# Kernel tuning notes

Hardware: AMD Instinct MI355X
Metric: run time of the kernel (lower is better)

The kernel has to match this reference:

```python
import jax, jax.numpy as jnp
import numpy as np

NUM_HEADS = 8


def _mab(Q, K, Wq, bq, Wk, bk, Wv, bv, Wo, bo):
    # MAB with ln=False, dropout=0 (eval). Scale is sqrt(dim_V), matching source.
    B, Lq, _ = Q.shape
    Lk = K.shape[1]
    Dv = Wq.shape[1]
    dh = Dv // NUM_HEADS
    q = (Q @ Wq + bq).reshape(B, Lq, NUM_HEADS, dh).transpose(0, 2, 1, 3)
    k = (K @ Wk + bk).reshape(B, Lk, NUM_HEADS, dh).transpose(0, 2, 1, 3)
    v = (K @ Wv + bv).reshape(B, Lk, NUM_HEADS, dh).transpose(0, 2, 1, 3)
    A = jax.nn.softmax(jnp.einsum('bhqd,bhkd->bhqk', q, k) / jnp.sqrt(jnp.float32(Dv)), axis=-1)
    O = (q + jnp.einsum('bhqk,bhkd->bhqd', A, v)).transpose(0, 2, 1, 3).reshape(B, Lq, Dv)
    return O + jax.nn.relu(O @ Wo + bo)


def _forward(x, adj, gin_W, gin_b, geW1, geb1, geW2, geb2,
             gnW1, gnb1, gnW2, gnb2, goW, gob, S,
             mWq, mbq, mWk, mbk, mWv, mbv, mWo, mbo, finW, finb):
    B, V, T, D = x.shape
    Hd = gin_W.shape[1]
    # --- GNN encoder (adj path) ---
    h = x.reshape(B, V, T * D) @ gin_W + gin_b            # [B,V,H]
    # edge_mlp first linear on cat([h_i,h_j]) == h@Wi (row) + h@Wj (col); avoids 2H concat
    Wi, Wj = geW1[:Hd], geW1[Hd:]
    pre = (h @ Wi)[:, :, None, :] + (h @ Wj)[:, None, :, :] + geb1   # [B,V,V,H]
    e = jax.nn.relu(jax.nn.relu(pre) @ geW2 + geb2)       # [B,V,V,H]
    agg = jnp.einsum('bijh,bij->bih', e, adj)             # mask * sum over j, fused
    node = jax.nn.relu(jax.nn.relu(agg @ gnW1 + gnb1) @ gnW2 + gnb2)
    enc = node @ goW + gob                                # [B,V,H]
    # --- decoder: PMA + SAB + SAB + Linear ---
    o = _mab(jnp.broadcast_to(S, (B,) + S.shape[1:]), enc,
             mWq[0], mbq[0], mWk[0], mbk[0], mWv[0], mbv[0], mWo[0], mbo[0])
    o = _mab(o, o, mWq[1], mbq[1], mWk[1], mbk[1], mWv[1], mbv[1], mWo[1], mbo[1])
    o = _mab(o, o, mWq[2], mbq[2], mWk[2], mbk[2], mWv[2], mbv[2], mWo[2], mbo[2])
    out = o @ finW + finb                                 # [B,num_slots,T*OD]
    return out.reshape(B, S.shape[1], T, finW.shape[1] // T)


def setup_inputs() -> dict:
    key = jax.random.key(0)
    ks = jax.random.split(key, 16)
    B, V, T, D = 4, 256, 12, 4
    H, NS, OD = 256, 16, 32

    def w(k, shape, s=0.02):
        return s * jax.random.normal(k, shape, jnp.float32)

    return {
        'x': jax.random.normal(ks[0], (B, V, T, D), jnp.float32),
        'adj': (jax.random.uniform(ks[1], (B, V, V)) > 0.5).astype(jnp.float32),
        'gin_W': w(ks[2], (T * D, H)), 'gin_b': jnp.zeros((H,), jnp.float32),
        'geW1': w(ks[3], (2 * H, H)), 'geb1': jnp.zeros((H,), jnp.float32),
        'geW2': w(ks[4], (H, H)), 'geb2': jnp.zeros((H,), jnp.float32),
        'gnW1': w(ks[5], (H, H)), 'gnb1': jnp.zeros((H,), jnp.float32),
        'gnW2': w(ks[6], (H, H)), 'gnb2': jnp.zeros((H,), jnp.float32),
        'goW': w(ks[7], (H, H)), 'gob': jnp.zeros((H,), jnp.float32),
        'S': w(ks[8], (1, NS, H), 0.05),
        'mWq': w(ks[9], (3, H, H)), 'mbq': jnp.zeros((3, H), jnp.float32),
        'mWk': w(ks[10], (3, H, H)), 'mbk': jnp.zeros((3, H), jnp.float32),
        'mWv': w(ks[11], (3, H, H)), 'mbv': jnp.zeros((3, H), jnp.float32),
        'mWo': w(ks[12], (3, H, H)), 'mbo': jnp.zeros((3, H), jnp.float32),
        'finW': w(ks[13], (H, T * OD)), 'finb': jnp.zeros((T * OD,), jnp.float32),
    }


def reference(x, adj, gin_W, gin_b, geW1, geb1, geW2, geb2,
              gnW1, gnb1, gnW2, gnb2, goW, gob, S,
              mWq, mbq, mWk, mbk, mWv, mbv, mWo, mbo, finW, finb):
    return _forward(x, adj, gin_W, gin_b, geW1, geb1, geW2, geb2,
                    gnW1, gnb1, gnW2, gnb2, goW, gob, S,
                    mWq, mbq, mWk, mbk, mWv, mbv, mWo, mbo, finW, finb)
```

## Files before the change

### kernel.cpp

```cpp
#include <hip/hip_runtime.h>
#include <hip/hip_bf16.h>

typedef unsigned short u16;
typedef __bf16 bf8v __attribute__((ext_vector_type(8)));
typedef float f4v __attribute__((ext_vector_type(4)));

__device__ __forceinline__ float b2f(u16 v) {
  union { unsigned u; float f; } x; x.u = ((unsigned)v) << 16; return x.f;
}
__device__ __forceinline__ u16 f2b(float f) {
  union { float f; unsigned u; } x; x.f = f;
  unsigned r = (x.u + 0x7FFFu + ((x.u >> 16) & 1u)) >> 16;
  return (u16)r;
}
__device__ __forceinline__ unsigned pkbf(float a, float b) {
  union { __hip_bfloat162 h; unsigned u; } c;
  c.h = __float22bfloat162_rn(make_float2(a, b));
  return c.u;
}
__device__ __forceinline__ void up2(unsigned u, float& lo, float& hi) {
  union { unsigned x; float f; } a, b;
  a.x = u << 16; b.x = u & 0xffff0000u; lo = a.f; hi = b.f;
}

#define NFRAG 19
struct PreArgs {
  const float* fsrc[NFRAG];
  u16* fdst[NFRAG];
  int fstride[NFRAG];
  int fbase[NFRAG + 1];
  int fragTiles, hBase, prepBid, q1Bid;
  const float *x, *ginW, *ginb;
  u16* h_bf;
  const float *mbk, *mbv, *mbq, *S, *mWq;
  float *bkv0, *bqkv1, *bqkv2;
  u16* q1b;
};

__global__ __launch_bounds__(256) void k_pre(PreArgs a) {
  __shared__ u16 ld[256 * 20];
  __shared__ float xs[4][48];
  __shared__ float Ss[4096];
  const int bid = blockIdx.x, t = threadIdx.x;

  if (bid < a.fragTiles) {
    int j = 0;
    while (j + 1 < NFRAG && a.fbase[j + 1] <= bid) j++;
    const int localT = bid - a.fbase[j];
    const float* src = a.fsrc[j];
    const int Ns = a.fstride[j];
    const int n0 = localT * 16;
    {
      const float* s = src + (size_t)t * Ns + n0;
      const float4 v0 = ((const float4*)s)[0], v1 = ((const float4*)s)[1];
      const float4 v2 = ((const float4*)s)[2], v3 = ((const float4*)s)[3];
      unsigned* row = (unsigned*)(ld + t * 20);
      row[0] = pkbf(v0.x, v0.y); row[1] = pkbf(v0.z, v0.w);
      row[2] = pkbf(v1.x, v1.y); row[3] = pkbf(v1.z, v1.w);
      row[4] = pkbf(v2.x, v2.y); row[5] = pkbf(v2.z, v2.w);
      row[6] = pkbf(v3.x, v3.y); row[7] = pkbf(v3.z, v3.w);
    }
    __syncthreads();
    u16* dst = a.fdst[j] + (size_t)localT * 4096;
#pragma unroll
    for (int s2 = 0; s2 < 2; s2++) {
      const int o = t * 2 + s2, kt = o >> 6, lane = o & 63;
      const int nlo = lane & 15, bk = kt * 32 + ((lane >> 4) << 3);
      union { u16 h[8]; uint4 q; } pk;
#pragma unroll
      for (int j2 = 0; j2 < 8; j2++) pk.h[j2] = ld[(bk + j2) * 20 + nlo];
      *(uint4*)(dst + (size_t)(kt * 64 + lane) * 8) = pk.q;
    }
    return;
  }
  if (bid >= a.hBase && bid < a.hBase + 256) {
    const int row0 = (bid - a.hBase) * 4;
    if (t < 192) {
      const int rr = t / 48, k = t % 48;
      xs[rr][k] = a.x[(size_t)(row0 + rr) * 48 + k];
    }
    __syncthreads();
    const float bias = a.ginb[t];
    float acc[4] = {bias, bias, bias, bias};
    for (int k = 0; k < 48; k++) {
      const float w = a.ginW[(size_t)k * 256 + t];
#pragma unroll
      for (int rr = 0; rr < 4; rr++) acc[rr] += xs[rr][k] * w;
    }
#pragma unroll
    for (int rr = 0; rr < 4; rr++) a.h_bf[(size_t)(row0 + rr) * 256 + t] = f2b(acc[rr]);
    return;
  }
  if (bid == a.prepBid) {
    a.bkv0[t] = a.mbk[t]; a.bkv0[256 + t] = a.mbv[t];
    a.bqkv1[t] = a.mbq[256 + t]; a.bqkv1[256 + t] = a.mbk[256 + t]; a.bqkv1[512 + t] = a.mbv[256 + t];
    a.bqkv2[t] = a.mbq[512 + t]; a.bqkv2[256 + t] = a.mbk[512 + t]; a.bqkv2[512 + t] = a.mbv[512 + t];
    return;
  }
  if (bid == a.q1Bid) {
    for (int idx = t; idx < 4096; idx += 256) Ss[idx] = a.S[idx];
    __syncthreads();
    float acc[16];
#pragma unroll
    for (int r = 0; r < 16; r++) acc[r] = 0.f;
    for (int k = 0; k < 256; k++) {
      const float w = a.mWq[(size_t)k * 256 + t];
#pragma unroll
      for (int r = 0; r < 16; r++) acc[r] += Ss[r * 256 + k] * w;
    }
    const float bq = a.mbq[t];
#pragma unroll
    for (int r = 0; r < 16; r++) a.q1b[r * 256 + t] = f2b(acc[r] + bq);
    return;
  }
}

__global__ __launch_bounds__(256) void k_wiwj(
    const u16* __restrict__ h, const u16* __restrict__ frag,
    float* __restrict__ hWiF, u16* __restrict__ hWjB) {
  __shared__ __align__(16) u16 As[64 * 264];
  const int t = threadIdx.x, lane = t & 63, wv = t >> 6;
  const int m0 = blockIdx.x * 64, n0 = blockIdx.y * 128;
  {
    const int row = t >> 2, ch = t & 3;
#pragma unroll
    for (int s = 0; s < 8; s++)
      *(uint4*)(As + row * 264 + ch * 64 + s * 8) =
          *(const uint4*)(h + (size_t)(m0 + row) * 256 + ch * 64 + s * 8);
  }
  __syncthreads();
  f4v acc[4][2];
#pragma unroll
  for (int mt = 0; mt < 4; mt++)
#pragma unroll
    for (int nt = 0; nt < 2; nt++) acc[mt][nt] = (f4v){0.f, 0.f, 0.f, 0.f};
  const int Tw = (n0 >> 4) + wv * 2;
#pragma unroll
  for (int kt = 0; kt < 8; kt++) {
    bf8v af[4], bf[2];
#pragma unroll
    for (int mt = 0; mt < 4; mt++)
      af[mt] = *(const bf8v*)(As + (mt * 16 + (lane & 15)) * 264 + kt * 32 + ((lane >> 4) << 3));
#pragma unroll
    for (int nt = 0; nt < 2; nt++)
      bf[nt] = *(const bf8v*)(frag + ((size_t)((Tw + nt) * 8 + kt) * 64 + lane) * 8);
#pragma unroll
    for (int mt = 0; mt < 4; mt++)
#pragma unroll
      for (int nt = 0; nt < 2; nt++)
        acc[mt][nt] = __builtin_amdgcn_mfma_f32_16x16x32_bf16(af[mt], bf[nt], acc[mt][nt], 0, 0, 0);
  }
#pragma unroll
  for (int mt = 0; mt < 4; mt++)
#pragma unroll
    for (int nt = 0; nt < 2; nt++) {
      const int n = n0 + wv * 32 + nt * 16 + (lane & 15);
      const int mb = m0 + mt * 16 + ((lane >> 4) << 2);
#pragma unroll
      for (int r = 0; r < 4; r++) {
        if (n < 256)
          hWiF[(size_t)(mb + r) * 256 + n] = acc[mt][nt][r];
        else
          hWjB[(size_t)(mb + r) * 256 + (n - 256)] = f2b(acc[mt][nt][r]);
      }
    }
}

__global__ __launch_bounds__(256) void k_edge(
    const float* __restrict__ hWiF, const u16* __restrict__ hWjB,
    const float* __restrict__ adj, const float* __restrict__ geb1,
    const u16* __restrict__ fragW2, const float* __restrict__ geb2,
    u16* __restrict__ aggB) {
  __shared__ __align__(16) u16 As[64 * 280];
  __shared__ float hi[256];
  __shared__ int jlist[256];
  __shared__ int cnt;
  const int t = threadIdx.x, lane = t & 63, wv = t >> 6;
  const int b = blockIdx.x >> 8, i = blockIdx.x & 255;
  if (t == 0) cnt = 0;
  __syncthreads();
  {
    const float a = adj[(size_t)(b * 256 + i) * 256 + t];
    hi[t] = hWiF[(size_t)(b * 256 + i) * 256 + t] + geb1[t];
    if (a != 0.f) { const int p = atomicAdd(&cnt, 1); jlist[p] = t; }
  }
  __syncthreads();
  const int nact = cnt;
  if (nact == 0) {
    if (lane < 16) {
#pragma unroll
      for (int nt = 0; nt < 4; nt++)
        aggB[(size_t)(b * 256 + i) * 256 + wv * 64 + nt * 16 + lane] = 0;
    }
    return;
  }
  const int nch = (nact + 63) >> 6;
  float bias2[4];
#pragma unroll
  for (int nt = 0; nt < 4; nt++) bias2[nt] = geb2[wv * 64 + nt * 16 + (lane & 15)];
  float aggAcc[4] = {0.f, 0.f, 0.f, 0.f};
  const u16* fw = fragW2 + lane * 8;
  const int r = t >> 2, q = t & 3;

  uint4 G[8];
  {
    const int rows0 = min(64, nact);
    const int j = (r < rows0) ? jlist[r] : jlist[0];
    const uint4* s4 = (const uint4*)(hWjB + (size_t)(b * 256 + j) * 256 + q * 64);
#pragma unroll
    for (int ii = 0; ii < 8; ii++) G[ii] = s4[ii];
  }

  for (int c = 0; c < nch; c++) {
    const int rows = min(64, nact - c * 64);
    {
      u16* dstrow = As + r * 280 + q * 72;
#pragma unroll
      for (int ii = 0; ii < 8; ii++) {
        const uint4 v = G[ii];
        const int k = q * 64 + ii * 8;
        float f0, f1, f2, f3, f4, f5, f6, f7;
        up2(v.x, f0, f1); up2(v.y, f2, f3); up2(v.z, f4, f5); up2(v.w, f6, f7);
        uint4 qd;
        qd.x = pkbf(fmaxf(f0 + hi[k + 0], 0.f), fmaxf(f1 + hi[k + 1], 0.f));
        qd.y = pkbf(fmaxf(f2 + hi[k + 2], 0.f), fmaxf(f3 + hi[k + 3], 0.f));
        qd.z = pkbf(fmaxf(f4 + hi[k + 4], 0.f), fmaxf(f5 + hi[k + 5], 0.f));
        qd.w = pkbf(fmaxf(f6 + hi[k + 6], 0.f), fmaxf(f7 + hi[k + 7], 0.f));
        *(uint4*)(dstrow + ii * 8) = qd;
      }
    }
    __syncthreads();
    if (c + 1 < nch) {
      const int rowsN = min(64, nact - (c + 1) * 64);
      const int j = (r < rowsN) ? jlist[(c + 1) * 64 + r] : jlist[0];
      const uint4* s4 = (const uint4*)(hWjB + (size_t)(b * 256 + j) * 256 + q * 64);
#pragma unroll
      for (int ii = 0; ii < 8; ii++) G[ii] = s4[ii];
    }
    f4v acc[4][4];
#pragma unroll
    for (int jt = 0; jt < 4; jt++)
#pragma unroll
      for (int nt = 0; nt < 4; nt++) acc[jt][nt] = (f4v){0.f, 0.f, 0.f, 0.f};
#pragma unroll
    for (int kt = 0; kt < 8; kt++) {
      bf8v af[4];
      const int coff = (kt >> 1) * 72 + (kt & 1) * 32 + ((lane >> 4) << 3);
#pragma unroll
      for (int jt = 0; jt < 4; jt++)
        af[jt] = *(const bf8v*)(As + (jt * 16 + (lane & 15)) * 280 + coff);
#pragma unroll
      for (int nt = 0; nt < 4; nt++) {
        const bf8v bw = *(const bf8v*)(fw + (size_t)((wv * 4 + nt) * 8 + kt) * 512);
#pragma unroll
        for (int jt = 0; jt < 4; jt++)
          acc[jt][nt] = __builtin_amdgcn_mfma_f32_16x16x32_bf16(af[jt], bw, acc[jt][nt], 0, 0, 0);
      }
    }
    const int rbase = (lane >> 4) * 4;
#pragma unroll
    for (int nt = 0; nt < 4; nt++) {
      float s = 0.f;
#pragma unroll
      for (int jt = 0; jt < 4; jt++) {
        const int r0 = jt * 16 + rbase;
#pragma unroll
        for (int rr = 0; rr < 4; rr++) {
          const float e = fmaxf(acc[jt][nt][rr] + bias2[nt], 0.f);
          s += (r0 + rr < rows) ? e : 0.f;
        }
      }
      s += __shfl_xor(s, 16);
      s += __shfl_xor(s, 32);
      aggAcc[nt] += s;
    }
    __syncthreads();
  }
  if (lane < 16) {
#pragma unroll
    for (int nt = 0; nt < 4; nt++) {
      const int n = wv * 64 + nt * 16 + lane;
      aggB[(size_t)(b * 256 + i) * 256 + n] = f2b(aggAcc[nt]);
    }
  }
}

#define NBLK 32

__device__ __forceinline__ void gridbar(int* cnt, int gen) {
  __syncthreads();
  if (threadIdx.x == 0) {
    __threadfence();
    __hip_atomic_fetch_add(cnt, 1, __ATOMIC_RELAXED, __HIP_MEMORY_SCOPE_AGENT);
    int it = 0;
    while (__hip_atomic_load(cnt, __ATOMIC_RELAXED, __HIP_MEMORY_SCOPE_AGENT) < NBLK * gen) {
      __builtin_amdgcn_s_sleep(8);
      if (((++it) & 255) == 0)
        __hip_atomic_fetch_add(cnt, 0, __ATOMIC_RELAXED, __HIP_MEMORY_SCOPE_AGENT);
    }
    __threadfence();
  }
  __syncthreads();
}

__device__ void g32(const u16* Al, const u16* frag, const float* bias, int relu,
                    u16* Ol, int t) {
  const int lane = t & 63, wv = t >> 6;
  f4v acc[2][4];
#pragma unroll
  for (int mt = 0; mt < 2; mt++)
#pragma unroll
    for (int nt = 0; nt < 4; nt++) acc[mt][nt] = (f4v){0.f, 0.f, 0.f, 0.f};
#pragma unroll
  for (int kt = 0; kt < 8; kt++) {
    bf8v af[2], bf[4];
#pragma unroll
    for (int mt = 0; mt < 2; mt++)
      af[mt] = *(const bf8v*)(Al + (mt * 16 + (lane & 15)) * 264 + kt * 32 + ((lane >> 4) << 3));
#pragma unroll
    for (int nt = 0; nt < 4; nt++)
      bf[nt] = *(const bf8v*)(frag + ((size_t)((wv * 4 + nt) * 8 + kt) * 64 + lane) * 8);
#pragma unroll
    for (int mt = 0; mt < 2; mt++)
#pragma unroll
      for (int nt = 0; nt < 4; nt++)
        acc[mt][nt] = __builtin_amdgcn_mfma_f32_16x16x32_bf16(af[mt], bf[nt], acc[mt][nt], 0, 0, 0);
  }
#pragma unroll
  for (int mt = 0; mt < 2; mt++)
#pragma unroll
    for (int nt = 0; nt < 4; nt++) {
      const int col = wv * 64 + nt * 16 + (lane & 15);
      const float bv = bias[col];
#pragma unroll
      for (int r = 0; r < 4; r++) {
        const int row = mt * 16 + ((lane >> 4) << 2) + r;
        float v = acc[mt][nt][r] + bv;
        if (relu) v = fmaxf(v, 0.f);
        Ol[row * 264 + col] = f2b(v);
      }
    }
}

__device__ void g32kv(const u16* Al, const u16* frag, const float* bias,
                      u16* outG, int t) {
  const int lane = t & 63, wv = t >> 6;
  f4v acc[2][8];
#pragma unroll
  for (int mt = 0; mt < 2; mt++)
#pragma unroll
    for (int nt = 0; nt < 8; nt++) acc[mt][nt] = (f4v){0.f, 0.f, 0.f, 0.f};
#pragma unroll
  for (int kt = 0; kt < 8; kt++) {
    bf8v af[2];
#pragma unroll
    for (int mt = 0; mt < 2; mt++)
      af[mt] = *(const bf8v*)(Al + (mt * 16 + (lane & 15)) * 264 + kt * 32 + ((lane >> 4) << 3));
#pragma unroll
    for (int nt = 0; nt < 8; nt++) {
      const bf8v bf = *(const bf8v*)(frag + ((size_t)((wv * 8 + nt) * 8 + kt) * 64 + lane) * 8);
#pragma unroll
      for (int mt = 0; mt < 2; mt++)
        acc[mt][nt] = __builtin_amdgcn_mfma_f32_16x16x32_bf16(af[mt], bf, acc[mt][nt], 0, 0, 0);
    }
  }
#pragma unroll
  for (int mt = 0; mt < 2; mt++)
#pragma unroll
    for (int nt = 0; nt < 8; nt++) {
      const int col = wv * 128 + nt * 16 + (lane & 15);
      const float bv = bias[col];
#pragma unroll
      for (int r = 0; r < 4; r++) {
        const int row = mt * 16 + ((lane >> 4) << 2) + r;
        outG[(size_t)row * 512 + col] = f2b(acc[mt][nt][r] + bv);
      }
    }
}

__device__ void attn_tile(const u16* __restrict__ qbuf,
                          const u16* __restrict__ kbuf, const u16* __restrict__ vbuf,
                          float* __restrict__ oF, u16* __restrict__ oB,
                          int b, int hd, float* qs, float* sc, float* vs, int t) {
  const int lane = t & 63, wv = t >> 6;
  const int Lk = 256;
  if (t < 64) {
    const int row = t >> 2, part = t & 3;
    const uint4 q4 = *(const uint4*)(qbuf + (size_t)row * 256 + hd * 32 + part * 8);
    float f0, f1, f2, f3, f4, f5, f6, f7;
    up2(q4.x, f0, f1); up2(q4.y, f2, f3); up2(q4.z, f4, f5); up2(q4.w, f6, f7);
    float4* d = (float4*)(qs + row * 32 + part * 8);
    d[0] = make_float4(f0, f1, f2, f3);
    d[1] = make_float4(f4, f5, f6, f7);
  }
  __syncthreads();
  {
    float kv[32];
    const uint4* kp = (const uint4*)(kbuf + (size_t)(b * Lk + t) * 512 + hd * 32);
#pragma unroll
    for (int c4 = 0; c4 < 4; c4++) {
      const uint4 k4 = kp[c4];
      up2(k4.x, kv[c4 * 8 + 0], kv[c4 * 8 + 1]);
      up2(k4.y, kv[c4 * 8 + 2], kv[c4 * 8 + 3]);
      up2(k4.z, kv[c4 * 8 + 4], kv[c4 * 8 + 5]);
      up2(k4.w, kv[c4 * 8 + 6], kv[c4 * 8 + 7]);
    }
    for (int r = 0; r < 16; r++) {
      float s = 0.f;
#pragma unroll
      for (int d = 0; d < 32; d++) s += qs[r * 32 + d] * kv[d];
      sc[r * 256 + t] = s * 0.0625f;
    }
  }
  __syncthreads();
  for (int r = wv * 4; r < wv * 4 + 4; r++) {
    float v[4];
    float mx = -1e30f;
#pragma unroll
    for (int q2 = 0; q2 < 4; q2++) {
      v[q2] = sc[r * 256 + lane + q2 * 64];
      mx = fmaxf(mx, v[q2]);
    }
    for (int off = 32; off; off >>= 1) mx = fmaxf(mx, __shfl_xor(mx, off));
    float sum = 0.f;
#pragma unroll
    for (int q2 = 0; q2 < 4; q2++) { v[q2] = __expf(v[q2] - mx); sum += v[q2]; }
    for (int off = 32; off; off >>= 1) sum += __shfl_xor(sum, off);
    const float inv = 1.f / sum;
#pragma unroll
    for (int q2 = 0; q2 < 4; q2++) sc[r * 256 + lane + q2 * 64] = v[q2] * inv;
  }
  __syncthreads();
  for (int u = t; u < 1024; u += 256) {
    const int row = u >> 2, part = u & 3;
    const uint4 v4 = *(const uint4*)(vbuf + (size_t)(b * Lk + row) * 512 + hd * 32 + part * 8);
    float f0, f1, f2, f3, f4, f5, f6, f7;
    up2(v4.x, f0, f1); up2(v4.y, f2, f3); up2(v4.z, f4, f5); up2(v4.w, f6, f7);
    float4* d = (float4*)(vs + row * 32 + part * 8);
    d[0] = make_float4(f0, f1, f2, f3);
    d[1] = make_float4(f4, f5, f6, f7);
  }
  __syncthreads();
  const int r0 = t >> 5, d = t & 31;
  float a0 = qs[r0 * 32 + d], a1 = qs[(r0 + 8) * 32 + d];
#pragma unroll 4
  for (int j = 0; j < Lk; j++) {
    const float vv = vs[j * 32 + d];
    a0 += sc[r0 * 256 + j] * vv;
    a1 += sc[(r0 + 8) * 256 + j] * vv;
  }
  const int c0 = hd * 32 + d;
  oF[(size_t)(b * 16 + r0) * 256 + c0] = a0;
  oB[(size_t)(b * 16 + r0) * 256 + c0] = f2b(a0);
  oF[(size_t)(b * 16 + r0 + 8) * 256 + c0] = a1;
  oB[(size_t)(b * 16 + r0 + 8) * 256 + c0] = f2b(a1);
}

__device__ void wprojG(const u16* __restrict__ o1b, const float* __restrict__ o1f,
                       const u16* __restrict__ frag, const float* __restrict__ bias,
                       u16* actL, float* residL, int b, int T, int lane) {
  f4v acc = (f4v){0.f, 0.f, 0.f, 0.f};
  const u16* abase = o1b + (size_t)(b * 16 + (lane & 15)) * 256 + ((lane >> 4) << 3);
  const u16* fbase = frag + ((size_t)(T * 8) * 64 + lane) * 8;
#pragma unroll
  for (int kt = 0; kt < 8; kt++)
    acc = __builtin_amdgcn_mfma_f32_16x16x32_bf16(*(const bf8v*)(abase + kt * 32),
                                                  *(const bf8v*)(fbase + (size_t)kt * 512), acc, 0, 0, 0);
  const int col = T * 16 + (lane & 15);
  const float bv = bias[col];
#pragma unroll
  for (int r = 0; r < 4; r++) {
    const int row = ((lane >> 4) << 2) + r;
    const float v = fmaxf(acc[r] + bv, 0.f) + o1f[(size_t)(b * 16 + row) * 256 + col];
    residL[row * 256 + col] = v;
    actL[row * 264 + col] = f2b(v);
  }
}

__device__ void wprojQ(const u16* actL, const u16* __restrict__ frag,
                       const float* __restrict__ bias, u16* qkvL, int T, int lane) {
  f4v acc = (f4v){0.f, 0.f, 0.f, 0.f};
  const u16* abase = actL + (lane & 15) * 264 + ((lane >> 4) << 3);
  const u16* fbase = frag + ((size_t)(T * 8) * 64 + lane) * 8;
#pragma unroll
  for (int kt = 0; kt < 8; kt++)
    acc = __builtin_amdgcn_mfma_f32_16x16x32_bf16(*(const bf8v*)(abase + kt * 32),
                                                  *(const bf8v*)(fbase + (size_t)kt * 512), acc, 0, 0, 0);
  const int col = T * 16 + (lane & 15);
  const float bv = bias[col];
#pragma unroll
  for (int r = 0; r < 4; r++) {
    const int row = ((lane >> 4) << 2) + r;
    qkvL[row * 776 + col] = f2b(acc[r] + bv);
  }
}

__device__ void wprojR(const u16* actIn, const u16* __restrict__ frag,
                       const float* __restrict__ bias, u16* actOut, float* residL,
                       int T, int lane) {
  f4v acc = (f4v){0.f, 0.f, 0.f, 0.f};
  const u16* abase = actIn + (lane & 15) * 264 + ((lane >> 4) << 3);
  const u16* fbase = frag + ((size_t)(T * 8) * 64 + lane) * 8;
#pragma unroll
  for (int kt = 0; kt < 8; kt++)
    acc = __builtin_amdgcn_mfma_f32_16x16x32_bf16(*(const bf8v*)(abase + kt * 32),
                                                  *(const bf8v*)(fbase + (size_t)kt * 512), acc, 0, 0, 0);
  const int col = T * 16 + (lane & 15);
  const float bv = bias[col];
#pragma unroll
  for (int r = 0; r < 4; r++) {
    const int row = ((lane >> 4) << 2) + r;
    const float v = fmaxf(acc[r] + bv, 0.f) + residL[row * 256 + col];
    residL[row * 256 + col] = v;
    actOut[row * 264 + col] = f2b(v);
  }
}

__device__ void wprojF(const u16* actL, const u16* __restrict__ frag,
                       const float* __restrict__ bias, float* __restrict__ outG,
                       int T, int lane) {
  f4v acc = (f4v){0.f, 0.f, 0.f, 0.f};
  const u16* abase = actL + (lane & 15) * 264 + ((lane >> 4) << 3);
  const u16* fbase = frag + ((size_t)(T * 8) * 64 + lane) * 8;
#pragma unroll
  for (int kt = 0; kt < 8; kt++)
    acc = __builtin_amdgcn_mfma_f32_16x16x32_bf16(*(const bf8v*)(abase + kt * 32),
                                                  *(const bf8v*)(fbase + (size_t)kt * 512), acc, 0, 0, 0);
  const int col = T * 16 + (lane & 15);
  const float bv = bias[col];
#pragma unroll
  for (int r = 0; r < 4; r++) {
    const int row = ((lane >> 4) << 2) + r;
    outG[(size_t)row * 384 + col] = acc[r] + bv;
  }
}

__device__ void attnB(const u16* qkvL, float* residL, u16* actOut, float* ps,
                      int hd, int lane) {
  const int r = lane & 15, cg = lane >> 4;
  float qv[32];
  {
    const uint4* qp = (const uint4*)(qkvL + r * 776 + hd * 32);
#pragma unroll
    for (int c4 = 0; c4 < 4; c4++) {
      const uint4 q4 = qp[c4];
      up2(q4.x, qv[c4 * 8 + 0], qv[c4 * 8 + 1]);
      up2(q4.y, qv[c4 * 8 + 2], qv[c4 * 8 + 3]);
      up2(q4.z, qv[c4 * 8 + 4], qv[c4 * 8 + 5]);
      up2(q4.w, qv[c4 * 8 + 6], qv[c4 * 8 + 7]);
    }
  }
  float p[4];
#pragma unroll
  for (int c = 0; c < 4; c++) {
    const int cc = cg * 4 + c;
    const uint4* kp = (const uint4*)(qkvL + cc * 776 + 256 + hd * 32);
    float s = 0.f;
#pragma unroll
    for (int c4 = 0; c4 < 4; c4++) {
      const uint4 k4 = kp[c4];
      float k0, k1;
      up2(k4.x, k0, k1); s += qv[c4 * 8 + 0] * k0 + qv[c4 * 8 + 1] * k1;
      up2(k4.y, k0, k1); s += qv[c4 * 8 + 2] * k0 + qv[c4 * 8 + 3] * k1;
      up2(k4.z, k0, k1); s += qv[c4 * 8 + 4] * k0 + qv[c4 * 8 + 5] * k1;
      up2(k4.w, k0, k1); s += qv[c4 * 8 + 6] * k0 + qv[c4 * 8 + 7] * k1;
    }
    p[c] = s * 0.0625f;
  }
  float mx = fmaxf(fmaxf(p[0], p[1]), fmaxf(p[2], p[3]));
  mx = fmaxf(mx, __shfl_xor(mx, 16));
  mx = fmaxf(mx, __shfl_xor(mx, 32));
  float sum = 0.f;
#pragma unroll
  for (int c = 0; c < 4; c++) { p[c] = __expf(p[c] - mx); sum += p[c]; }
  sum += __shfl_xor(sum, 16);
  sum += __shfl_xor(sum, 32);
  const float inv = 1.f / sum;
#pragma unroll
  for (int c = 0; c < 4; c++) ps[r * 16 + cg * 4 + c] = p[c] * inv;
  float o[8];
#pragma unroll
  for (int j = 0; j < 8; j++) o[j] = qv[cg * 8 + j];
#pragma unroll
  for (int c = 0; c < 16; c++) {
    const float pv = ps[r * 16 + c];
    const uint4 v4 = *(const uint4*)(qkvL + c * 776 + 512 + hd * 32 + cg * 8);
    float v0, v1;
    up2(v4.x, v0, v1); o[0] += pv * v0; o[1] += pv * v1;
    up2(v4.y, v0, v1); o[2] += pv * v0; o[3] += pv * v1;
    up2(v4.z, v0, v1); o[4] += pv * v0; o[5] += pv * v1;
    up2(v4.w, v0, v1); o[6] += pv * v0; o[7] += pv * v1;
  }
  const int col0 = hd * 32 + cg * 8;
#pragma unroll
  for (int j = 0; j < 8; j++) residL[r * 256 + col0 + j] = o[j];
  unsigned* ob = (unsigned*)(actOut + r * 264 + col0);
  ob[0] = pkbf(o[0], o[1]); ob[1] = pkbf(o[2], o[3]);
  ob[2] = pkbf(o[4], o[5]); ob[3] = pkbf(o[6], o[7]);
}

struct TailArgs {
  const u16 *agg, *fGn1, *fGn2, *fGo, *fKV0, *fQKV1, *fQKV2, *fO0, *fO1, *fO2, *fFin, *q1b;
  const float *gnb1, *gnb2, *gob, *bkv0, *bqkv1, *bqkv2, *mbo, *finb;
  u16 *kv1, *o1b;
  float *o1f, *outF;
  int* bar;
};

__global__ __launch_bounds__(256) void k_tail(TailArgs a) {
  __shared__ __align__(16) char smem[62208];
  const int bid = blockIdx.x, t = threadIdx.x;
  const int lane = t & 63, w = t >> 6;

  {
    u16* actA = (u16*)smem;
    u16* actB = (u16*)(smem + 16896);
    const int r0 = bid * 32;
#pragma unroll
    for (int s = 0; s < 4; s++) {
      const int u = t * 4 + s, row = u >> 5, ch = u & 31;
      *(uint4*)(actA + row * 264 + ch * 8) =
          *(const uint4*)(a.agg + (size_t)(r0 + row) * 256 + ch * 8);
    }
    __syncthreads();
    g32(actA, a.fGn1, a.gnb1, 1, actB, t); __syncthreads();
    g32(actB, a.fGn2, a.gnb2, 1, actA, t); __syncthreads();
    g32(actA, a.fGo, a.gob, 0, actB, t); __syncthreads();
    g32kv(actB, a.fKV0, a.bkv0, a.kv1 + (size_t)r0 * 512, t);
  }
  gridbar(a.bar, 1);
  {
    float* qs = (float*)smem;
    float* sc = (float*)(smem + 2048);
    float* vs = (float*)(smem + 18432);
    attn_tile(a.q1b, a.kv1, a.kv1 + 256, a.o1f, a.o1b, bid >> 3, bid & 7, qs, sc, vs, t);
  }
  gridbar(a.bar, 2);
  if (bid >= 4) return;
  {
    const int b = bid;
    u16* act0 = (u16*)smem;
    u16* act1 = (u16*)(smem + 8448);
    u16* qkvL = (u16*)(smem + 16896);
    float* residL = (float*)(smem + 41728);
    float* psL = (float*)(smem + 58112);
    __syncthreads();
    for (int T = w; T < 16; T += 4) wprojG(a.o1b, a.o1f, a.fO0, a.mbo, act0, residL, b, T, lane);
    __syncthreads();
    for (int T = w; T < 48; T += 4) wprojQ(act0, a.fQKV1, a.bqkv1, qkvL, T, lane);
    __syncthreads();
    for (int hd = w; hd < 8; hd += 4) attnB(qkvL, residL, act1, psL + w * 256, hd, lane);
    __syncthreads();
    for (int T = w; T < 16; T += 4) wprojR(act1, a.fO1, a.mbo + 256, act0, residL, T, lane);
    __syncthreads();
    for (int T = w; T < 48; T += 4) wprojQ(act0, a.fQKV2, a.bqkv2, qkvL, T, lane);
    __syncthreads();
    for (int hd = w; hd < 8; hd += 4) attnB(qkvL, residL, act1, psL + w * 256, hd, lane);
    __syncthreads();
    for (int T = w; T < 16; T += 4) wprojR(act1, a.fO2, a.mbo + 512, act0, residL, T, lane);
    __syncthreads();
    for (int T = w; T < 24; T += 4)
      wprojF(act0, a.fFin, a.finb, a.outF + (size_t)b * 16 * 384, T, lane);
  }
}

extern "C" void kernel_launch(void* const* d_in, const int* in_sizes, int n_in,
                              void* d_out, int out_size, void* d_ws, size_t ws_size,
                              hipStream_t stream) {
  const float* x    = (const float*)d_in[0];
  const float* adj  = (const float*)d_in[1];
  const float* ginW = (const float*)d_in[2];
  const float* ginb = (const float*)d_in[3];
  const float* geW1 = (const float*)d_in[4];
  const float* geb1 = (const float*)d_in[5];
  const float* geW2 = (const float*)d_in[6];
  const float* geb2 = (const float*)d_in[7];
  const float* gnW1 = (const float*)d_in[8];
  const float* gnb1 = (const float*)d_in[9];
  const float* gnW2 = (const float*)d_in[10];
  const float* gnb2 = (const float*)d_in[11];
  const float* goW  = (const float*)d_in[12];
  const float* gob  = (const float*)d_in[13];
  const float* S    = (const float*)d_in[14];
  const float* mWq  = (const float*)d_in[15];
  const float* mbq  = (const float*)d_in[16];
  const float* mWk  = (const float*)d_in[17];
  const float* mbk  = (const float*)d_in[18];
  const float* mWv  = (const float*)d_in[19];
  const float* mbv  = (const float*)d_in[20];
  const float* mWo  = (const float*)d_in[21];
  const float* mbo  = (const float*)d_in[22];
  const float* finW = (const float*)d_in[23];
  const float* finb = (const float*)d_in[24];
  (void)in_sizes; (void)n_in; (void)out_size; (void)ws_size;

  char* wp = (char*)d_ws;
  size_t off = 0;
  auto alloc = [&](size_t bytes) -> char* {
    char* p = wp + off;
    off += (bytes + 255) & ~(size_t)255;
    return p;
  };
  u16* h_bf     = (u16*)alloc(1024 * 256 * 2);
  float* hWiF   = (float*)alloc((size_t)1024 * 256 * 4);
  u16* hWjB     = (u16*)alloc(1024 * 256 * 2);
  u16* fWiWj    = (u16*)alloc(512 * 256 * 2);
  u16* fW2      = (u16*)alloc(256 * 256 * 2);
  u16* fGn1     = (u16*)alloc(256 * 256 * 2);
  u16* fGn2     = (u16*)alloc(256 * 256 * 2);
  u16* fGo      = (u16*)alloc(256 * 256 * 2);
  u16* fQ0      = (u16*)alloc(256 * 256 * 2);
  u16* fKV0     = (u16*)alloc(512 * 256 * 2);
  u16* fQKV1    = (u16*)alloc(768 * 256 * 2);
  u16* fQKV2    = (u16*)alloc(768 * 256 * 2);
  u16* fO0      = (u16*)alloc(256 * 256 * 2);
  u16* fO1      = (u16*)alloc(256 * 256 * 2);
  u16* fO2      = (u16*)alloc(256 * 256 * 2);
  u16* fFin     = (u16*)alloc(384 * 256 * 2);
  float* bkv0   = (float*)alloc(512 * 4);
  float* bqkv1  = (float*)alloc(768 * 4);
  float* bqkv2  = (float*)alloc(768 * 4);
  u16* q1b      = (u16*)alloc(16 * 256 * 2);
  u16* agg_b    = (u16*)alloc(1024 * 256 * 2);
  u16* kv1      = (u16*)alloc(1024 * 512 * 2);
  float* o1f    = (float*)alloc(64 * 256 * 4);
  u16* o1b      = (u16*)alloc(64 * 256 * 2);
  int* bar      = (int*)alloc(256);

  PreArgs P{};
  int nj = 0, tiles = 0;
  auto addF = [&](const float* s, int stride, u16* d, int nT) {
    P.fsrc[nj] = s; P.fdst[nj] = d; P.fstride[nj] = stride; P.fbase[nj] = tiles;
    tiles += nT; nj++;
  };
  addF(geW1, 256, fWiWj, 16);
  addF(geW1 + 65536, 256, fWiWj + 16 * 4096, 16);
  addF(geW2, 256, fW2, 16);
  addF(gnW1, 256, fGn1, 16);
  addF(gnW2, 256, fGn2, 16);
  addF(goW, 256, fGo, 16);
  addF(mWq, 256, fQ0, 16);
  addF(mWk, 256, fKV0, 16);
  addF(mWv, 256, fKV0 + 16 * 4096, 16);
  addF(mWq + 65536, 256, fQKV1, 16);
  addF(mWk + 65536, 256, fQKV1 + 16 * 4096, 16);
  addF(mWv + 65536, 256, fQKV1 + 32 * 4096, 16);
  addF(mWq + 131072, 256, fQKV2, 16);
  addF(mWk + 131072, 256, fQKV2 + 16 * 4096, 16);
  addF(mWv + 131072, 256, fQKV2 + 32 * 4096, 16);
  addF(mWo, 256, fO0, 16);
  addF(mWo + 65536, 256, fO1, 16);
  addF(mWo + 131072, 256, fO2, 16);
  addF(finW, 384, fFin, 24);
  P.fbase[nj] = tiles;
  P.fragTiles = tiles;
  P.hBase = tiles;
  P.prepBid = tiles + 256;
  P.q1Bid = tiles + 257;
  P.x = x; P.ginW = ginW; P.ginb = ginb; P.h_bf = h_bf;
  P.mbk = mbk; P.mbv = mbv; P.mbq = mbq; P.S = S; P.mWq = mWq;
  P.bkv0 = bkv0; P.bqkv1 = bqkv1; P.bqkv2 = bqkv2; P.q1b = q1b;

  TailArgs T{};
  T.agg = agg_b; T.fGn1 = fGn1; T.fGn2 = fGn2; T.fGo = fGo; T.fKV0 = fKV0;
  T.fQKV1 = fQKV1; T.fQKV2 = fQKV2; T.fO0 = fO0; T.fO1 = fO1; T.fO2 = fO2;
  T.fFin = fFin; T.q1b = q1b;
  T.gnb1 = gnb1; T.gnb2 = gnb2; T.gob = gob;
  T.bkv0 = bkv0; T.bqkv1 = bqkv1; T.bqkv2 = bqkv2; T.mbo = mbo; T.finb = finb;
  T.kv1 = kv1; T.o1b = o1b; T.o1f = o1f; T.outF = (float*)d_out;
  T.bar = bar;

  hipMemsetAsync(bar, 0, 256, stream);
  k_pre<<<dim3(tiles + 258), dim3(256), 0, stream>>>(P);
  k_wiwj<<<dim3(16, 4), dim3(256), 0, stream>>>(h_bf, fWiWj, hWiF, hWjB);
  k_edge<<<dim3(1024), dim3(256), 0, stream>>>(hWiF, hWjB, adj, geb1, fW2, geb2, agg_b);
  k_tail<<<dim3(NBLK), dim3(256), 0, stream>>>(T);
}
```

Before: 262.0 us.

## Fuse input projection and Wi/Wj GEMM into the weight-prep kernel

Merges the gin input linear and the h@Wi/h@Wj GEMM into the first kernel, eliminating the separate k_wiwj launch and the h_bf intermediate buffer. The 64 new blocks recompute h for their 64-row tile in shared memory and read geW1 directly from fp32 global memory, converting it to bf16 on the fly instead of using pre-packed fragments. The unused fQ0 and geW1 fragment prep is dropped. In exchange, each row tile's h is recomputed by 4 blocks, B operand loads are strided and uncoalesced, and there is 46KB of shared memory per block.

```diff
diff --git a/kernel.cpp b/kernel.cpp
--- a/kernel.cpp
+++ b/kernel.cpp
@@ -23,30 +23,106 @@
   a.x = u << 16; b.x = u & 0xffff0000u; lo = a.f; hi = b.f;
 }
 
-#define NFRAG 19
-struct PreArgs {
+#define NFRAG 16
+struct HeadArgs {
   const float* fsrc[NFRAG];
   u16* fdst[NFRAG];
   int fstride[NFRAG];
   int fbase[NFRAG + 1];
-  int fragTiles, hBase, prepBid, q1Bid;
-  const float *x, *ginW, *ginb;
-  u16* h_bf;
+  int fragTiles, prepBid, q1Bid;
+  const float *x, *ginW, *ginb, *geW1;
+  float* hWiF;
+  u16* hWjB;
   const float *mbk, *mbv, *mbq, *S, *mWq;
   float *bkv0, *bqkv1, *bqkv2;
   u16* q1b;
 };
 
-__global__ __launch_bounds__(256) void k_pre(PreArgs a) {
-  __shared__ u16 ld[256 * 20];
-  __shared__ float xs[4][48];
-  __shared__ float Ss[4096];
+__global__ __launch_bounds__(256) void k_head(HeadArgs a) {
+  __shared__ __align__(16) char sm[46080];
   const int bid = blockIdx.x, t = threadIdx.x;
 
-  if (bid < a.fragTiles) {
+  if (bid < 64) {
+    u16* As = (u16*)sm;
+    float* xs = (float*)(sm + 33792);
+    const int lane = t & 63, wv = t >> 6;
+    const int m0 = (bid >> 2) * 64, n0 = (bid & 3) * 128;
+    for (int idx = t; idx < 64 * 48; idx += 256)
+      xs[idx] = a.x[(size_t)(m0 + idx / 48) * 48 + idx % 48];
+    __syncthreads();
+    {
+      float w48[48];
+#pragma unroll
+      for (int k = 0; k < 48; k++) w48[k] = a.ginW[(size_t)k * 256 + t];
+      const float bias = a.ginb[t];
+      for (int rg = 0; rg < 16; rg++) {
+        float acc[4] = {bias, bias, bias, bias};
+#pragma unroll
+        for (int k = 0; k < 48; k++) {
+          const float w = w48[k];
+#pragma unroll
+          for (int r = 0; r < 4; r++) acc[r] += xs[(rg * 4 + r) * 48 + k] * w;
+        }
+#pragma unroll
+        for (int r = 0; r < 4; r++) As[(rg * 4 + r) * 264 + t] = f2b(acc[r]);
+      }
+    }
+    __syncthreads();
+    f4v acc[4][2];
+#pragma unroll
+    for (int mt = 0; mt < 4; mt++)
+#pragma unroll
+      for (int nt = 0; nt < 2; nt++) acc[mt][nt] = (f4v){0.f, 0.f, 0.f, 0.f};
+#pragma unroll
+    for (int kt = 0; kt < 8; kt++) {
+      bf8v af[4], bf[2];
+#pragma unroll
+      for (int mt = 0; mt < 4; mt++)
+        af[mt] = *(const bf8v*)(As + (mt * 16 + (lane & 15)) * 264 + kt * 32 + ((lane >> 4) << 3));
+#pragma unroll
+      for (int nt = 0; nt < 2; nt++) {
+        const int n = n0 + wv * 32 + nt * 16 + (lane & 15);
+        const int kb = kt * 32 + ((lane >> 4) << 3);
+        const float* wsrc = (n < 256)
+            ? (a.geW1 + (size_t)kb * 256 + n)
+            : (a.geW1 + (size_t)(256 + kb) * 256 + (n - 256));
+        float f[8];
+#pragma unroll
+        for (int j = 0; j < 8; j++) f[j] = wsrc[(size_t)j * 256];
+        union { unsigned u[4]; bf8v v; } bb;
+        bb.u[0] = pkbf(f[0], f[1]); bb.u[1] = pkbf(f[2], f[3]);
+        bb.u[2] = pkbf(f[4], f[5]); bb.u[3] = pkbf(f[6], f[7]);
+        bf[nt] = bb.v;
+      }
+#pragma unroll
+      for (int mt = 0; mt < 4; mt++)
+#pragma unroll
+        for (int nt = 0; nt < 2; nt++)
+          acc[mt][nt] = __builtin_amdgcn_mfma_f32_16x16x32_bf16(af[mt], bf[nt], acc[mt][nt], 0, 0, 0);
+    }
+#pragma unroll
+    for (int mt = 0; mt < 4; mt++)
+#pragma unroll
+      for (int nt = 0; nt < 2; nt++) {
+        const int n = n0 + wv * 32 + nt * 16 + (lane & 15);
+        const int mb = m0 + mt * 16 + ((lane >> 4) << 2);
+#pragma unroll
+        for (int r = 0; r < 4; r++) {
+          if (n < 256)
+            a.hWiF[(size_t)(mb + r) * 256 + n] = acc[mt][nt][r];
+          else
+            a.hWjB[(size_t)(mb + r) * 256 + (n - 256)] = f2b(acc[mt][nt][r]);
+        }
+      }
+    return;
+  }
+
+  const int pb = bid - 64;
+  if (pb < a.fragTiles) {
+    u16* ld = (u16*)sm;
     int j = 0;
-    while (j + 1 < NFRAG && a.fbase[j + 1] <= bid) j++;
-    const int localT = bid - a.fbase[j];
+    while (j + 1 < NFRAG && a.fbase[j + 1] <= pb) j++;
+    const int localT = pb - a.fbase[j];
     const float* src = a.fsrc[j];
     const int Ns = a.fstride[j];
     const int n0 = localT * 16;
@@ -73,24 +149,6 @@
     }
     return;
   }
-  if (bid >= a.hBase && bid < a.hBase + 256) {
-    const int row0 = (bid - a.hBase) * 4;
-    if (t < 192) {
-      const int rr = t / 48, k = t % 48;
-      xs[rr][k] = a.x[(size_t)(row0 + rr) * 48 + k];
-    }
-    __syncthreads();
-    const float bias = a.ginb[t];
-    float acc[4] = {bias, bias, bias, bias};
-    for (int k = 0; k < 48; k++) {
-      const float w = a.ginW[(size_t)k * 256 + t];
-#pragma unroll
-      for (int rr = 0; rr < 4; rr++) acc[rr] += xs[rr][k] * w;
-    }
-#pragma unroll
-    for (int rr = 0; rr < 4; rr++) a.h_bf[(size_t)(row0 + rr) * 256 + t] = f2b(acc[rr]);
-    return;
-  }
   if (bid == a.prepBid) {
     a.bkv0[t] = a.mbk[t]; a.bkv0[256 + t] = a.mbv[t];
     a.bqkv1[t] = a.mbq[256 + t]; a.bqkv1[256 + t] = a.mbk[256 + t]; a.bqkv1[512 + t] = a.mbv[256 + t];
@@ -98,6 +156,7 @@
     return;
   }
   if (bid == a.q1Bid) {
+    float* Ss = (float*)sm;
     for (int idx = t; idx < 4096; idx += 256) Ss[idx] = a.S[idx];
     __syncthreads();
     float acc[16];
@@ -113,57 +172,6 @@
     for (int r = 0; r < 16; r++) a.q1b[r * 256 + t] = f2b(acc[r] + bq);
     return;
   }
-}
-
-__global__ __launch_bounds__(256) void k_wiwj(
-    const u16* __restrict__ h, const u16* __restrict__ frag,
-    float* __restrict__ hWiF, u16* __restrict__ hWjB) {
-  __shared__ __align__(16) u16 As[64 * 264];
-  const int t = threadIdx.x, lane = t & 63, wv = t >> 6;
-  const int m0 = blockIdx.x * 64, n0 = blockIdx.y * 128;
-  {
-    const int row = t >> 2, ch = t & 3;
-#pragma unroll
-    for (int s = 0; s < 8; s++)
-      *(uint4*)(As + row * 264 + ch * 64 + s * 8) =
-          *(const uint4*)(h + (size_t)(m0 + row) * 256 + ch * 64 + s * 8);
-  }
-  __syncthreads();
-  f4v acc[4][2];
-#pragma unroll
-  for (int mt = 0; mt < 4; mt++)
-#pragma unroll
-    for (int nt = 0; nt < 2; nt++) acc[mt][nt] = (f4v){0.f, 0.f, 0.f, 0.f};
-  const int Tw = (n0 >> 4) + wv * 2;
-#pragma unroll
-  for (int kt = 0; kt < 8; kt++) {
-    bf8v af[4], bf[2];
-#pragma unroll
-    for (int mt = 0; mt < 4; mt++)
-      af[mt] = *(const bf8v*)(As + (mt * 16 + (lane & 15)) * 264 + kt * 32 + ((lane >> 4) << 3));
-#pragma unroll
-    for (int nt = 0; nt < 2; nt++)
-      bf[nt] = *(const bf8v*)(frag + ((size_t)((Tw + nt) * 8 + kt) * 64 + lane) * 8);
-#pragma unroll
-    for (int mt = 0; mt < 4; mt++)
-#pragma unroll
-      for (int nt = 0; nt < 2; nt++)
-        acc[mt][nt] = __builtin_amdgcn_mfma_f32_16x16x32_bf16(af[mt], bf[nt], acc[mt][nt], 0, 0, 0);
-  }
-#pragma unroll
-  for (int mt = 0; mt < 4; mt++)
-#pragma unroll
-    for (int nt = 0; nt < 2; nt++) {
-      const int n = n0 + wv * 32 + nt * 16 + (lane & 15);
-      const int mb = m0 + mt * 16 + ((lane >> 4) << 2);
-#pragma unroll
-      for (int r = 0; r < 4; r++) {
-        if (n < 256)
-          hWiF[(size_t)(mb + r) * 256 + n] = acc[mt][nt][r];
-        else
-          hWjB[(size_t)(mb + r) * 256 + (n - 256)] = f2b(acc[mt][nt][r]);
-      }
-    }
 }
 
 __global__ __launch_bounds__(256) void k_edge(
@@ -701,15 +709,12 @@
     off += (bytes + 255) & ~(size_t)255;
     return p;
   };
-  u16* h_bf     = (u16*)alloc(1024 * 256 * 2);
   float* hWiF   = (float*)alloc((size_t)1024 * 256 * 4);
   u16* hWjB     = (u16*)alloc(1024 * 256 * 2);
-  u16* fWiWj    = (u16*)alloc(512 * 256 * 2);
   u16* fW2      = (u16*)alloc(256 * 256 * 2);
   u16* fGn1     = (u16*)alloc(256 * 256 * 2);
   u16* fGn2     = (u16*)alloc(256 * 256 * 2);
   u16* fGo      = (u16*)alloc(256 * 256 * 2);
-  u16* fQ0      = (u16*)alloc(256 * 256 * 2);
   u16* fKV0     = (u16*)alloc(512 * 256 * 2);
   u16* fQKV1    = (u16*)alloc(768 * 256 * 2);
   u16* fQKV2    = (u16*)alloc(768 * 256 * 2);
@@ -727,19 +732,16 @@
   u16* o1b      = (u16*)alloc(64 * 256 * 2);
   int* bar      = (int*)alloc(256);
 
-  PreArgs P{};
+  HeadArgs H{};
   int nj = 0, tiles = 0;
   auto addF = [&](const float* s, int stride, u16* d, int nT) {
-    P.fsrc[nj] = s; P.fdst[nj] = d; P.fstride[nj] = stride; P.fbase[nj] = tiles;
+    H.fsrc[nj] = s; H.fdst[nj] = d; H.fstride[nj] = stride; H.fbase[nj] = tiles;
     tiles += nT; nj++;
   };
-  addF(geW1, 256, fWiWj, 16);
-  addF(geW1 + 65536, 256, fWiWj + 16 * 4096, 16);
   addF(geW2, 256, fW2, 16);
   addF(gnW1, 256, fGn1, 16);
   addF(gnW2, 256, fGn2, 16);
   addF(goW, 256, fGo, 16);
-  addF(mWq, 256, fQ0, 16);
   addF(mWk, 256, fKV0, 16);
   addF(mWv, 256, fKV0 + 16 * 4096, 16);
   addF(mWq + 65536, 256, fQKV1, 16);
@@ -752,14 +754,14 @@
   addF(mWo + 65536, 256, fO1, 16);
   addF(mWo + 131072, 256, fO2, 16);
   addF(finW, 384, fFin, 24);
-  P.fbase[nj] = tiles;
-  P.fragTiles = tiles;
-  P.hBase = tiles;
-  P.prepBid = tiles + 256;
-  P.q1Bid = tiles + 257;
-  P.x = x; P.ginW = ginW; P.ginb = ginb; P.h_bf = h_bf;
-  P.mbk = mbk; P.mbv = mbv; P.mbq = mbq; P.S = S; P.mWq = mWq;
-  P.bkv0 = bkv0; P.bqkv1 = bqkv1; P.bqkv2 = bqkv2; P.q1b = q1b;
+  H.fbase[nj] = tiles;
+  H.fragTiles = tiles;
+  H.prepBid = 64 + tiles;
+  H.q1Bid = 64 + tiles + 1;
+  H.x = x; H.ginW = ginW; H.ginb = ginb; H.geW1 = geW1;
+  H.hWiF = hWiF; H.hWjB = hWjB;
+  H.mbk = mbk; H.mbv = mbv; H.mbq = mbq; H.S = S; H.mWq = mWq;
+  H.bkv0 = bkv0; H.bqkv1 = bqkv1; H.bqkv2 = bqkv2; H.q1b = q1b;
 
   TailArgs T{};
   T.agg = agg_b; T.fGn1 = fGn1; T.fGn2 = fGn2; T.fGo = fGo; T.fKV0 = fKV0;
@@ -771,8 +773,7 @@
   T.bar = bar;
 
   hipMemsetAsync(bar, 0, 256, stream);
-  k_pre<<<dim3(tiles + 258), dim3(256), 0, stream>>>(P);
-  k_wiwj<<<dim3(16, 4), dim3(256), 0, stream>>>(h_bf, fWiWj, hWiF, hWjB);
+  k_head<<<dim3(64 + tiles + 2), dim3(256), 0, stream>>>(H);
   k_edge<<<dim3(1024), dim3(256), 0, stream>>>(hWiF, hWjB, adj, geb1, fW2, geb2, agg_b);
   k_tail<<<dim3(NBLK), dim3(256), 0, stream>>>(T);
 }
```

Result: no change. 259.7 us (-0.9%).
